# Kernel optimization log

Hardware: AMD Instinct MI355X
Metric: run time of the kernel (lower is better)

The kernel has to match this reference:

```python
import jax, jax.numpy as jnp
from jax import lax
import numpy as np


def conv4d(x, w, b, pad):
    """4D conv (stride 1) as a sum of 3D convs over the first-spatial-dim kernel taps.
    x: [B, Cin, T, D, H, W]; w: [Cout, Cin, Kt, Kd, Kh, Kw]; same pad on all dims."""
    B, Cin, T, D, H, W = x.shape
    Cout, _, Kt = w.shape[:3]
    xp = jnp.pad(x, ((0, 0), (0, 0), (pad, pad), (0, 0), (0, 0), (0, 0)))
    Tout = T + 2 * pad - Kt + 1
    acc = None
    for k in range(Kt):  # loop over kernel taps (<=3), not data dims
        xs = xp[:, :, k:k + Tout]                      # [B,Cin,Tout,D,H,W]
        xs = xs.transpose(0, 2, 1, 3, 4, 5).reshape(B * Tout, Cin, D, H, W)
        y = lax.conv_general_dilated(
            xs, w[:, :, k], (1, 1, 1), [(pad, pad)] * 3,
            dimension_numbers=('NCDHW', 'OIDHW', 'NCDHW'))
        acc = y if acc is None else acc + y
    Do, Ho, Wo = acc.shape[2:]
    out = acc.reshape(B, Tout, Cout, Do, Ho, Wo).transpose(0, 2, 1, 3, 4, 5)
    return out + b[None, :, None, None, None, None]


def tconv4d_k2s2(x, w, b):
    """4D transposed conv, kernel=2, stride=2, pad=0 (non-overlapping blocks).
    x: [B,Cin,T,D,H,W]; w: [Cin,Cout,2,2,2,2] (PyTorch ConvTranspose layout)."""
    B, Cin, T, D, H, W = x.shape
    Cout = w.shape[1]
    y = jnp.einsum('bcijkl,copqrs->boipjqkrls', x, w)
    y = y.reshape(B, Cout, 2 * T, 2 * D, 2 * H, 2 * W)
    return y + b[None, :, None, None, None, None]


def setup_inputs() -> dict:
    key = jax.random.key(0)
    ks = jax.random.split(key, 10)
    Cin, Cout = 64, 32
    x1 = jax.random.normal(ks[0], (2, Cin, 8, 8, 8, 8), dtype=jnp.float32)
    x2 = jax.random.normal(ks[1], (2, Cin // 2, 16, 16, 16, 16), dtype=jnp.float32)
    def w(k, shape, fan_in):
        return jax.random.normal(k, shape, dtype=jnp.float32) / np.float32(np.sqrt(fan_in))
    up_w = w(ks[2], (Cin, Cin // 2, 2, 2, 2, 2), Cin * 16)
    up_b = w(ks[3], (Cin // 2,), Cin * 16)
    w1 = w(ks[4], (Cout, Cin, 3, 3, 3, 3), Cin * 81)
    b1 = w(ks[5], (Cout,), Cin * 81)
    w2 = w(ks[6], (Cout, Cout, 3, 3, 3, 3), Cout * 81)
    b2 = w(ks[7], (Cout,), Cout * 81)
    w3 = w(ks[8], (Cout, Cin, 1, 1, 1, 1), Cin)
    b3 = w(ks[9], (Cout,), Cin)
    return {'x1': x1, 'x2': x2, 'up_w': up_w, 'up_b': up_b,
            'w1': w1, 'b1': b1, 'w2': w2, 'b2': b2, 'w3': w3, 'b3': b3}


def reference(x1, x2, up_w, up_b, w1, b1, w2, b2, w3, b3):
    x1u = tconv4d_k2s2(x1, up_w, up_b)              # [B, Cin//2, 16,16,16,16]
    xc = jnp.concatenate([x2, x1u], axis=1)          # [B, Cin, 16,16,16,16]
    Y = jax.nn.relu(conv4d(xc, w1, b1, 1))
    Y = conv4d(Y, w2, b2, 1)
    sc = conv4d(xc, w3, b3, 0)                       # 1x1 residual projection
    return jax.nn.relu(Y + sc)
```

## Files before the change

### kernel.cpp

```cpp
#include <hip/hip_runtime.h>

typedef unsigned short u16;
typedef __attribute__((ext_vector_type(8))) short short8;
typedef __attribute__((ext_vector_type(4))) float f32x4;

#define XCB_OFF  0
#define Y1B_OFF  8388608
#define W1P_OFF  12582912
#define W2P_OFF  12748800
#define W3P_OFF  12831744
#define UPWP_OFF 12833792

__device__ __forceinline__ u16 f2bf(float v) {
    unsigned u = __builtin_bit_cast(unsigned, v);
    u += 0x7FFFu + ((u >> 16) & 1u);
    return (u16)(u >> 16);
}

__device__ __forceinline__ f32x4 MFMA(short8 a, short8 b, f32x4 c) {
    return __builtin_amdgcn_mfma_f32_16x16x32_bf16(a, b, c, 0, 0, 0);
}

__device__ __forceinline__ void decode_bid(int bid, int& b, int& t, int& d, int& h0) {
    int xcd = bid & 7, loc = bid >> 3;
    int hB = loc & 1;
    d = (loc >> 1) & 15;
    int tsub = (loc >> 5) & 1;
    b = loc >> 6;
    t = xcd * 2 + tsub;
    h0 = hB * 8;
}

__global__ __launch_bounds__(256) void setup(const float* __restrict__ w1,
                                             const float* __restrict__ w2,
                                             const float* __restrict__ w3,
                                             const float* __restrict__ upw,
                                             const float* __restrict__ x2,
                                             u16* __restrict__ ws) {
    __shared__ u16 lds[256 * 40];
    int bid = blockIdx.x;
    int tid = threadIdx.x;
    if (bid < 512) {
        int b = bid >> 8;
        int pos_base = (bid & 255) * 256;
        u16* xcb = ws + XCB_OFF;
        #pragma unroll
        for (int c = 0; c < 32; ++c) {
            lds[tid * 40 + c] = f2bf(x2[((b * 32 + c) << 16) + pos_base + tid]);
        }
        __syncthreads();
        #pragma unroll
        for (int k = 0; k < 4; ++k) {
            int f = k * 256 + tid;
            int u = f & 3, pos = f >> 2;
            uint4 v = *(const uint4*)(lds + pos * 40 + u * 8);
            *(uint4*)(xcb + (size_t)((b << 16) + pos_base + pos) * 64 + u * 8) = v;
        }
    } else {
        int idx = (bid - 512) * 256 + tid;
        if (idx < 165888) {
            int j = idx & 7, lane = (idx >> 3) & 63, rest = idx >> 9;
            int half = rest & 1, chunk = (rest >> 1) & 1, tap = rest >> 2;
            int co = half * 16 + (lane & 15), ci = chunk * 32 + (lane >> 4) * 8 + j;
            ws[W1P_OFF + idx] = f2bf(w1[(co * 64 + ci) * 81 + tap]);
        } else if (idx < 165888 + 82944) {
            int i2 = idx - 165888;
            int j = i2 & 7, lane = (i2 >> 3) & 63, rest = i2 >> 9;
            int half = rest & 1, tap = rest >> 1;
            int co = half * 16 + (lane & 15), ci = (lane >> 4) * 8 + j;
            ws[W2P_OFF + i2] = f2bf(w2[(co * 32 + ci) * 81 + tap]);
        } else if (idx < 165888 + 82944 + 2048) {
            int i3 = idx - (165888 + 82944);
            int j = i3 & 7, lane = (i3 >> 3) & 63, rest = i3 >> 9;
            int half = rest & 1, chunk = rest >> 1;
            int co = half * 16 + (lane & 15), ci = chunk * 32 + (lane >> 4) * 8 + j;
            ws[W3P_OFF + i3] = f2bf(w3[co * 64 + ci]);
        } else if (idx < 250880 + 32768) {
            int i4 = idx - 250880;
            int j = i4 & 7, lane = (i4 >> 3) & 63, rest = i4 >> 9;
            int half = rest & 1, chunk = (rest >> 1) & 1, tap = rest >> 2;
            int co = half * 16 + (lane & 15), ci = chunk * 32 + (lane >> 4) * 8 + j;
            ws[UPWP_OFF + i4] = f2bf(upw[(ci * 32 + co) * 16 + tap]);
        }
    }
}

__global__ __launch_bounds__(256) void xc_up_mfma(const float* __restrict__ x1,
                                                  const u16* __restrict__ upwp,
                                                  const float* __restrict__ up_b,
                                                  u16* __restrict__ xcb) {
    __shared__ u16 lds[64 * 72];
    int tid = threadIdx.x;
    int wv = tid >> 6, lane = tid & 63;
    int q = lane >> 4, m = lane & 15;
    int bid = blockIdx.x;
    int j = bid & 63, b = bid >> 6;
    int pos_base = j * 64;

    #pragma unroll
    for (int g = 0; g < 16; ++g) {
        int c = g * 4 + wv;
        lds[lane * 72 + c] = f2bf(x1[((b * 64 + c) << 12) + pos_base + lane]);
    }
    __syncthreads();

    const short8* wv8 = (const short8*)upwp;
    float4 bi0 = ((const float4*)up_b)[q];
    float4 bi1 = ((const float4*)up_b)[4 + q];
    int it = j >> 3, id = j & 7;

    for (int tt = 0; tt < 4; ++tt) {
        int tap = wv * 4 + tt;
        f32x4 acc[4][2];
        #pragma unroll
        for (int g = 0; g < 4; ++g) {
            acc[g][0] = (f32x4){bi0.x, bi0.y, bi0.z, bi0.w};
            acc[g][1] = (f32x4){bi1.x, bi1.y, bi1.z, bi1.w};
        }
        #pragma unroll
        for (int chunk = 0; chunk < 2; ++chunk) {
            short8 a0 = wv8[((tap * 2 + chunk) * 2 + 0) * 64 + lane];
            short8 a1 = wv8[((tap * 2 + chunk) * 2 + 1) * 64 + lane];
            #pragma unroll
            for (int g = 0; g < 4; ++g) {
                short8 bf = *(const short8*)(lds + (g * 16 + m) * 72 + chunk * 32 + q * 8);
                acc[g][0] = MFMA(a0, bf, acc[g][0]);
                acc[g][1] = MFMA(a1, bf, acc[g][1]);
            }
        }
        int pt = tap >> 3, pd = (tap >> 2) & 1, ph = (tap >> 1) & 1, pw = tap & 1;
        int oT = 2 * it + pt, oD = 2 * id + pd, oW = 2 * (m & 7) + pw;
        #pragma unroll
        for (int g = 0; g < 4; ++g) {
            int ih = g * 2 + (m >> 3);
            int opos = oT * 4096 + oD * 256 + (2 * ih + ph) * 16 + oW;
            u16* op = xcb + (size_t)((b << 16) + opos) * 64 + 32 + q * 4;
            #pragma unroll
            for (int half = 0; half < 2; ++half) {
                f32x4 v = acc[g][half];
                uint2 o;
                o.x = (unsigned)f2bf(v.x) | ((unsigned)f2bf(v.y) << 16);
                o.y = (unsigned)f2bf(v.z) | ((unsigned)f2bf(v.w) << 16);
                *(uint2*)(op + half * 16) = o;
            }
        }
    }
}

__global__ __launch_bounds__(256, 4) void conv1_mfma(const u16* __restrict__ xcb,
                                                     const u16* __restrict__ w1p,
                                                     const float* __restrict__ b1,
                                                     u16* __restrict__ y1b) {
    __shared__ u16 lds[11520];
    int tid = threadIdx.x;
    int lane = tid & 63, wv = tid >> 6;
    int q = lane >> 4, m = lane & 15;
    int c = wv & 1, rg = wv >> 1;
    int b, t, d, h0;
    decode_bid(blockIdx.x, b, t, d, h0);
    int rot = (blockIdx.x * 5) % 9;

    int lofs[6], gofs[6];
    bool st[6], inr[6];
    #pragma unroll
    for (int k = 0; k < 6; ++k) {
        int ui = tid + k * 256;
        int u = ui & 7, p = (ui >> 3) % 18, hh = ui / 144;
        int gh = h0 - 1 + hh, gw = p - 1;
        st[k] = ui < 1440;
        inr[k] = st[k] && ((unsigned)gh < 16u) && ((unsigned)gw < 16u);
        gofs[k] = (gh * 16 + gw) * 64 + u * 8;
        lofs[k] = hh * 1152 + p * 64 + ((u ^ (p & 7)) * 8);
    }

    f32x4 acc[4][2];
    if (c == 0) {
        float4 bi0 = ((const float4*)b1)[q];
        float4 bi1 = ((const float4*)b1)[4 + q];
        #pragma unroll
        for (int i = 0; i < 4; ++i) {
            acc[i][0] = (f32x4){bi0.x, bi0.y, bi0.z, bi0.w};
            acc[i][1] = (f32x4){bi1.x, bi1.y, bi1.z, bi1.w};
        }
    } else {
        #pragma unroll
        for (int i = 0; i < 4; ++i) {
            acc[i][0] = (f32x4){0.f, 0.f, 0.f, 0.f};
            acc[i][1] = (f32x4){0.f, 0.f, 0.f, 0.f};
        }
    }
    const short8* w1v = (const short8*)w1p;

    uint4 rP[6];
    auto load_plane = [&](int ktd) {
        int kt = ktd / 3, kd = ktd - kt * 3;
        int tt = t + kt - 1, dd = d + kd - 1;
        bool pv = ((unsigned)tt < 16u) && ((unsigned)dd < 16u);
        const u16* src = xcb + (size_t)(((b * 16 + tt) * 16 + dd)) * 16384;
        #pragma unroll
        for (int k = 0; k < 6; ++k) {
            uint4 v = {0, 0, 0, 0};
            if (pv && inr[k]) v = *(const uint4*)(src + gofs[k]);
            rP[k] = v;
        }
    };
    auto write_plane = [&]() {
        #pragma unroll
        for (int k = 0; k < 6; ++k)
            if (st[k]) *(uint4*)(lds + lofs[k]) = rP[k];
    };

    load_plane(rot);
    for (int s = 0; s < 9; ++s) {
        int ktd = rot + s; if (ktd >= 9) ktd -= 9;
        __syncthreads();
        write_plane();
        if (s < 8) {
            int nk = ktd + 1; if (nk >= 9) nk -= 9;
            load_plane(nk);
        }
        __syncthreads();
        __builtin_amdgcn_s_setprio(1);
        #pragma unroll
        for (int kw = 0; kw < 3; ++kw) {
            int p = kw + m, pm = p & 7;
            int bo = p * 64 + ((((c << 2) | q) ^ pm) << 3);
            short8 R[6];
            #pragma unroll
            for (int r = 0; r < 6; ++r)
                R[r] = *(const short8*)(lds + (rg * 4 + r) * 1152 + bo);
            #pragma unroll
            for (int kh = 0; kh < 3; ++kh) {
                int tap = (ktd * 3 + kh) * 3 + kw;
                short8 a0 = w1v[((tap * 2 + c) * 2 + 0) * 64 + lane];
                short8 a1 = w1v[((tap * 2 + c) * 2 + 1) * 64 + lane];
                #pragma unroll
                for (int i = 0; i < 4; ++i) {
                    acc[i][0] = MFMA(a0, R[i + kh], acc[i][0]);
                    acc[i][1] = MFMA(a1, R[i + kh], acc[i][1]);
                }
            }
        }
        __builtin_amdgcn_s_setprio(0);
    }

    __syncthreads();
    f32x4* buf = (f32x4*)lds;
    if (c == 1) {
        #pragma unroll
        for (int i = 0; i < 4; ++i)
            #pragma unroll
            for (int half = 0; half < 2; ++half)
                buf[((rg * 4 + i) * 2 + half) * 64 + lane] = acc[i][half];
    }
    __syncthreads();
    if (c == 0) {
        int obase = ((b * 16 + t) * 16 + d) * 256 + (h0 + rg * 4) * 16 + m;
        #pragma unroll
        for (int i = 0; i < 4; ++i) {
            int pos = obase + i * 16;
            #pragma unroll
            for (int half = 0; half < 2; ++half) {
                f32x4 v = acc[i][half];
                f32x4 w = buf[((rg * 4 + i) * 2 + half) * 64 + lane];
                v.x += w.x; v.y += w.y; v.z += w.z; v.w += w.w;
                unsigned r0 = f2bf(fmaxf(v.x, 0.f)), r1 = f2bf(fmaxf(v.y, 0.f));
                unsigned r2 = f2bf(fmaxf(v.z, 0.f)), r3 = f2bf(fmaxf(v.w, 0.f));
                uint2 o;
                o.x = r0 | (r1 << 16);
                o.y = r2 | (r3 << 16);
                *(uint2*)(y1b + (size_t)pos * 32 + half * 16 + q * 4) = o;
            }
        }
    }
}

__global__ __launch_bounds__(256, 4) void conv2_mfma(const u16* __restrict__ y1b,
                                                     const u16* __restrict__ xcb,
                                                     const u16* __restrict__ w2p,
                                                     const u16* __restrict__ w3p,
                                                     const float* __restrict__ b2,
                                                     const float* __restrict__ b3,
                                                     float* __restrict__ out) {
    __shared__ u16 lds[11520];
    int tid = threadIdx.x;
    int lane = tid & 63, wv = tid >> 6;
    int q = lane >> 4, m = lane & 15;
    int rg = wv;
    int b, t, d, h0;
    decode_bid(blockIdx.x, b, t, d, h0);
    int rot = (blockIdx.x * 5) % 9;

    int lofs[3], gofs[3];
    bool st[3], inr[3];
    #pragma unroll
    for (int k = 0; k < 3; ++k) {
        int ui = tid + k * 256;
        int u = ui & 3, p = (ui >> 2) % 18, hh = ui / 72;
        int gh = h0 - 1 + hh, gw = p - 1;
        st[k] = ui < 720;
        inr[k] = st[k] && ((unsigned)gh < 16u) && ((unsigned)gw < 16u);
        gofs[k] = (gh * 16 + gw) * 32 + u * 8;
        lofs[k] = hh * 576 + p * 32 + ((u ^ (p & 3)) * 8);
    }

    f32x4 acc[2][2];
    #pragma unroll
    for (int hf = 0; hf < 2; ++hf) {
        float4 p0 = ((const float4*)b2)[hf * 4 + q];
        float4 s0 = ((const float4*)b3)[hf * 4 + q];
        #pragma unroll
        for (int i = 0; i < 2; ++i)
            acc[i][hf] = (f32x4){p0.x + s0.x, p0.y + s0.y, p0.z + s0.z, p0.w + s0.w};
    }
    const short8* w2v = (const short8*)w2p;

    uint4 rP[3];
    auto load_plane = [&](int ktd) {
        int kt = ktd / 3, kd = ktd - kt * 3;
        int tt = t + kt - 1, dd = d + kd - 1;
        bool pv = ((unsigned)tt < 16u) && ((unsigned)dd < 16u);
        const u16* src = y1b + (size_t)(((b * 16 + tt) * 16 + dd)) * 8192;
        #pragma unroll
        for (int k = 0; k < 3; ++k) {
            uint4 v = {0, 0, 0, 0};
            if (pv && inr[k]) v = *(const uint4*)(src + gofs[k]);
            rP[k] = v;
        }
    };
    auto write_plane = [&](int bb) {
        #pragma unroll
        for (int k = 0; k < 3; ++k)
            if (st[k]) *(uint4*)(lds + bb * 5760 + lofs[k]) = rP[k];
    };

    load_plane(rot);
    write_plane(0);
    { int nk = rot + 1; if (nk >= 9) nk -= 9; load_plane(nk); }

    for (int s = 0; s < 9; ++s) {
        int ktd = rot + s; if (ktd >= 9) ktd -= 9;
        __syncthreads();
        const u16* L = lds + (s & 1) * 5760;
        __builtin_amdgcn_s_setprio(1);
        #pragma unroll
        for (int kw = 0; kw < 3; ++kw) {
            int p = kw + m, pm = p & 3;
            int bo = p * 32 + ((q ^ pm) << 3);
            short8 R[4];
            #pragma unroll
            for (int r = 0; r < 4; ++r)
                R[r] = *(const short8*)(L + (rg * 2 + r) * 576 + bo);
            #pragma unroll
            for (int kh = 0; kh < 3; ++kh) {
                int tap = (ktd * 3 + kh) * 3 + kw;
                short8 a0 = w2v[(tap * 2 + 0) * 64 + lane];
                short8 a1 = w2v[(tap * 2 + 1) * 64 + lane];
                #pragma unroll
                for (int i = 0; i < 2; ++i) {
                    acc[i][0] = MFMA(a0, R[i + kh], acc[i][0]);
                    acc[i][1] = MFMA(a1, R[i + kh], acc[i][1]);
                }
            }
        }
        __builtin_amdgcn_s_setprio(0);
        if (s < 8) {
            write_plane((s + 1) & 1);
            if (s < 7) {
                int nk = ktd + 2; if (nk >= 9) nk -= 9;
                load_plane(nk);
            }
        }
    }

    const short8* w3v = (const short8*)w3p;
    int lpos0 = (t * 16 + d) * 256 + (h0 + rg * 2) * 16 + m;
    int gpos0 = (b << 16) + lpos0;
    #pragma unroll
    for (int chunk = 0; chunk < 2; ++chunk) {
        short8 a0 = w3v[(chunk * 2 + 0) * 64 + lane];
        short8 a1 = w3v[(chunk * 2 + 1) * 64 + lane];
        #pragma unroll
        for (int i = 0; i < 2; ++i) {
            short8 bf = *(const short8*)(xcb + (size_t)(gpos0 + i * 16) * 64 + ((chunk << 2) | q) * 8);
            acc[i][0] = MFMA(a0, bf, acc[i][0]);
            acc[i][1] = MFMA(a1, bf, acc[i][1]);
        }
    }

    #pragma unroll
    for (int i = 0; i < 2; ++i) {
        int lpos = lpos0 + i * 16;
        #pragma unroll
        for (int hf = 0; hf < 2; ++hf) {
            f32x4 v = acc[i][hf];
            int co = hf * 16 + q * 4;
            float* op = out + (((size_t)(b * 32 + co)) << 16) + lpos;
            op[0ull << 16] = fmaxf(v.x, 0.f);
            op[1ull << 16] = fmaxf(v.y, 0.f);
            op[2ull << 16] = fmaxf(v.z, 0.f);
            op[3ull << 16] = fmaxf(v.w, 0.f);
        }
    }
}

extern "C" void kernel_launch(void* const* d_in, const int* in_sizes, int n_in,
                              void* d_out, int out_size, void* d_ws, size_t ws_size,
                              hipStream_t stream) {
    const float* x1   = (const float*)d_in[0];
    const float* x2   = (const float*)d_in[1];
    const float* up_w = (const float*)d_in[2];
    const float* up_b = (const float*)d_in[3];
    const float* w1   = (const float*)d_in[4];
    const float* b1   = (const float*)d_in[5];
    const float* w2   = (const float*)d_in[6];
    const float* b2   = (const float*)d_in[7];
    const float* w3   = (const float*)d_in[8];
    const float* b3   = (const float*)d_in[9];
    u16* ws  = (u16*)d_ws;
    float* out = (float*)d_out;

    setup<<<1620, 256, 0, stream>>>(w1, w2, w3, up_w, x2, ws);
    xc_up_mfma<<<128, 256, 0, stream>>>(x1, ws + UPWP_OFF, up_b, ws + XCB_OFF);
    conv1_mfma<<<1024, 256, 0, stream>>>(ws + XCB_OFF, ws + W1P_OFF, b1, ws + Y1B_OFF);
    conv2_mfma<<<1024, 256, 0, stream>>>(ws + Y1B_OFF, ws + XCB_OFF, ws + W2P_OFF,
                                         ws + W3P_OFF, b2, b3, out);
}
```

Baseline: 162.2 us.

## Shrink conv blocks to two waves with larger per-wave output tiles

```diff
diff --git a/kernel.cpp b/kernel.cpp
--- a/kernel.cpp
+++ b/kernel.cpp
@@ -147,24 +147,23 @@
     }
 }
 
-__global__ __launch_bounds__(256, 4) void conv1_mfma(const u16* __restrict__ xcb,
+__global__ __launch_bounds__(128, 2) void conv1_mfma(const u16* __restrict__ xcb,
                                                      const u16* __restrict__ w1p,
                                                      const float* __restrict__ b1,
                                                      u16* __restrict__ y1b) {
     __shared__ u16 lds[11520];
     int tid = threadIdx.x;
-    int lane = tid & 63, wv = tid >> 6;
+    int lane = tid & 63, c = tid >> 6;
     int q = lane >> 4, m = lane & 15;
-    int c = wv & 1, rg = wv >> 1;
     int b, t, d, h0;
     decode_bid(blockIdx.x, b, t, d, h0);
     int rot = (blockIdx.x * 5) % 9;
 
-    int lofs[6], gofs[6];
-    bool st[6], inr[6];
-    #pragma unroll
-    for (int k = 0; k < 6; ++k) {
-        int ui = tid + k * 256;
+    int lofs[12], gofs[12];
+    bool st[12], inr[12];
+    #pragma unroll
+    for (int k = 0; k < 12; ++k) {
+        int ui = tid + k * 128;
         int u = ui & 7, p = (ui >> 3) % 18, hh = ui / 144;
         int gh = h0 - 1 + hh, gw = p - 1;
         st[k] = ui < 1440;
@@ -173,32 +172,32 @@
         lofs[k] = hh * 1152 + p * 64 + ((u ^ (p & 7)) * 8);
     }
 
-    f32x4 acc[4][2];
+    f32x4 acc[8][2];
     if (c == 0) {
         float4 bi0 = ((const float4*)b1)[q];
         float4 bi1 = ((const float4*)b1)[4 + q];
         #pragma unroll
-        for (int i = 0; i < 4; ++i) {
+        for (int i = 0; i < 8; ++i) {
             acc[i][0] = (f32x4){bi0.x, bi0.y, bi0.z, bi0.w};
             acc[i][1] = (f32x4){bi1.x, bi1.y, bi1.z, bi1.w};
         }
     } else {
         #pragma unroll
-        for (int i = 0; i < 4; ++i) {
+        for (int i = 0; i < 8; ++i) {
             acc[i][0] = (f32x4){0.f, 0.f, 0.f, 0.f};
             acc[i][1] = (f32x4){0.f, 0.f, 0.f, 0.f};
         }
     }
     const short8* w1v = (const short8*)w1p;
 
-    uint4 rP[6];
+    uint4 rP[12];
     auto load_plane = [&](int ktd) {
         int kt = ktd / 3, kd = ktd - kt * 3;
         int tt = t + kt - 1, dd = d + kd - 1;
         bool pv = ((unsigned)tt < 16u) && ((unsigned)dd < 16u);
         const u16* src = xcb + (size_t)(((b * 16 + tt) * 16 + dd)) * 16384;
         #pragma unroll
-        for (int k = 0; k < 6; ++k) {
+        for (int k = 0; k < 12; ++k) {
             uint4 v = {0, 0, 0, 0};
             if (pv && inr[k]) v = *(const uint4*)(src + gofs[k]);
             rP[k] = v;
@@ -206,7 +205,7 @@
     };
     auto write_plane = [&]() {
         #pragma unroll
-        for (int k = 0; k < 6; ++k)
+        for (int k = 0; k < 12; ++k)
             if (st[k]) *(uint4*)(lds + lofs[k]) = rP[k];
     };
 
@@ -225,17 +224,17 @@
         for (int kw = 0; kw < 3; ++kw) {
             int p = kw + m, pm = p & 7;
             int bo = p * 64 + ((((c << 2) | q) ^ pm) << 3);
-            short8 R[6];
-            #pragma unroll
-            for (int r = 0; r < 6; ++r)
-                R[r] = *(const short8*)(lds + (rg * 4 + r) * 1152 + bo);
+            short8 R[10];
+            #pragma unroll
+            for (int r = 0; r < 10; ++r)
+                R[r] = *(const short8*)(lds + r * 1152 + bo);
             #pragma unroll
             for (int kh = 0; kh < 3; ++kh) {
                 int tap = (ktd * 3 + kh) * 3 + kw;
                 short8 a0 = w1v[((tap * 2 + c) * 2 + 0) * 64 + lane];
                 short8 a1 = w1v[((tap * 2 + c) * 2 + 1) * 64 + lane];
                 #pragma unroll
-                for (int i = 0; i < 4; ++i) {
+                for (int i = 0; i < 8; ++i) {
                     acc[i][0] = MFMA(a0, R[i + kh], acc[i][0]);
                     acc[i][1] = MFMA(a1, R[i + kh], acc[i][1]);
                 }
@@ -248,21 +247,21 @@
     f32x4* buf = (f32x4*)lds;
     if (c == 1) {
         #pragma unroll
-        for (int i = 0; i < 4; ++i)
+        for (int i = 0; i < 8; ++i)
             #pragma unroll
             for (int half = 0; half < 2; ++half)
-                buf[((rg * 4 + i) * 2 + half) * 64 + lane] = acc[i][half];
+                buf[(i * 2 + half) * 64 + lane] = acc[i][half];
     }
     __syncthreads();
     if (c == 0) {
-        int obase = ((b * 16 + t) * 16 + d) * 256 + (h0 + rg * 4) * 16 + m;
-        #pragma unroll
-        for (int i = 0; i < 4; ++i) {
+        int obase = ((b * 16 + t) * 16 + d) * 256 + h0 * 16 + m;
+        #pragma unroll
+        for (int i = 0; i < 8; ++i) {
             int pos = obase + i * 16;
             #pragma unroll
             for (int half = 0; half < 2; ++half) {
                 f32x4 v = acc[i][half];
-                f32x4 w = buf[((rg * 4 + i) * 2 + half) * 64 + lane];
+                f32x4 w = buf[(i * 2 + half) * 64 + lane];
                 v.x += w.x; v.y += w.y; v.z += w.z; v.w += w.w;
                 unsigned r0 = f2bf(fmaxf(v.x, 0.f)), r1 = f2bf(fmaxf(v.y, 0.f));
                 unsigned r2 = f2bf(fmaxf(v.z, 0.f)), r3 = f2bf(fmaxf(v.w, 0.f));
@@ -275,113 +274,111 @@
     }
 }
 
-__global__ __launch_bounds__(256, 4) void conv2_mfma(const u16* __restrict__ y1b,
+__global__ __launch_bounds__(128, 2) void conv2_mfma(const u16* __restrict__ y1b,
                                                      const u16* __restrict__ xcb,
                                                      const u16* __restrict__ w2p,
                                                      const u16* __restrict__ w3p,
                                                      const float* __restrict__ b2,
                                                      const float* __restrict__ b3,
                                                      float* __restrict__ out) {
-    __shared__ u16 lds[11520];
+    __shared__ u16 lds[10368];
     int tid = threadIdx.x;
-    int lane = tid & 63, wv = tid >> 6;
+    int lane = tid & 63, rg = tid >> 6;
     int q = lane >> 4, m = lane & 15;
-    int rg = wv;
-    int b, t, d, h0;
-    decode_bid(blockIdx.x, b, t, d, h0);
-    int rot = (blockIdx.x * 5) % 9;
-
-    int lofs[3], gofs[3];
-    bool st[3], inr[3];
-    #pragma unroll
-    for (int k = 0; k < 3; ++k) {
-        int ui = tid + k * 256;
+    int bid = blockIdx.x;
+    int xcd = bid & 7, loc = bid >> 3;
+    int d = loc & 15;
+    int tsub = (loc >> 4) & 1;
+    int b = loc >> 5;
+    int t = xcd * 2 + tsub;
+    int rot = (bid * 5) % 9;
+
+    int lofs[11], gofs[11];
+    bool st[11], inr[11];
+    #pragma unroll
+    for (int k = 0; k < 11; ++k) {
+        int ui = tid + k * 128;
         int u = ui & 3, p = (ui >> 2) % 18, hh = ui / 72;
-        int gh = h0 - 1 + hh, gw = p - 1;
-        st[k] = ui < 720;
+        int gh = hh - 1, gw = p - 1;
+        st[k] = ui < 1296;
         inr[k] = st[k] && ((unsigned)gh < 16u) && ((unsigned)gw < 16u);
         gofs[k] = (gh * 16 + gw) * 32 + u * 8;
         lofs[k] = hh * 576 + p * 32 + ((u ^ (p & 3)) * 8);
     }
 
-    f32x4 acc[2][2];
+    f32x4 acc[8][2];
     #pragma unroll
     for (int hf = 0; hf < 2; ++hf) {
         float4 p0 = ((const float4*)b2)[hf * 4 + q];
         float4 s0 = ((const float4*)b3)[hf * 4 + q];
         #pragma unroll
-        for (int i = 0; i < 2; ++i)
+        for (int i = 0; i < 8; ++i)
             acc[i][hf] = (f32x4){p0.x + s0.x, p0.y + s0.y, p0.z + s0.z, p0.w + s0.w};
     }
     const short8* w2v = (const short8*)w2p;
 
-    uint4 rP[3];
+    uint4 rP[11];
     auto load_plane = [&](int ktd) {
         int kt = ktd / 3, kd = ktd - kt * 3;
         int tt = t + kt - 1, dd = d + kd - 1;
         bool pv = ((unsigned)tt < 16u) && ((unsigned)dd < 16u);
         const u16* src = y1b + (size_t)(((b * 16 + tt) * 16 + dd)) * 8192;
         #pragma unroll
-        for (int k = 0; k < 3; ++k) {
+        for (int k = 0; k < 11; ++k) {
             uint4 v = {0, 0, 0, 0};
             if (pv && inr[k]) v = *(const uint4*)(src + gofs[k]);
             rP[k] = v;
         }
     };
-    auto write_plane = [&](int bb) {
-        #pragma unroll
-        for (int k = 0; k < 3; ++k)
-            if (st[k]) *(uint4*)(lds + bb * 5760 + lofs[k]) = rP[k];
+    auto write_plane = [&]() {
+        #pragma unroll
+        for (int k = 0; k < 11; ++k)
+            if (st[k]) *(uint4*)(lds + lofs[k]) = rP[k];
     };
 
     load_plane(rot);
-    write_plane(0);
-    { int nk = rot + 1; if (nk >= 9) nk -= 9; load_plane(nk); }
-
     for (int s = 0; s < 9; ++s) {
         int ktd = rot + s; if (ktd >= 9) ktd -= 9;
         __syncthreads();
-        const u16* L = lds + (s & 1) * 5760;
+        write_plane();
+        if (s < 8) {
+            int nk = ktd + 1; if (nk >= 9) nk -= 9;
+            load_plane(nk);
+        }
+        __syncthreads();
         __builtin_amdgcn_s_setprio(1);
         #pragma unroll
         for (int kw = 0; kw < 3; ++kw) {
             int p = kw + m, pm = p & 3;
             int bo = p * 32 + ((q ^ pm) << 3);
-            short8 R[4];
-            #pragma unroll
-            for (int r = 0; r < 4; ++r)
-                R[r] = *(const short8*)(L + (rg * 2 + r) * 576 + bo);
+            short8 R[10];
+            #pragma unroll
+            for (int r = 0; r < 10; ++r)
+                R[r] = *(const short8*)(lds + (rg * 8 + r) * 576 + bo);
             #pragma unroll
             for (int kh = 0; kh < 3; ++kh) {
                 int tap = (ktd * 3 + kh) * 3 + kw;
                 short8 a0 = w2v[(tap * 2 + 0) * 64 + lane];
                 short8 a1 = w2v[(tap * 2 + 1) * 64 + lane];
                 #pragma unroll
-                for (int i = 0; i < 2; ++i) {
+                for (int i = 0; i < 8; ++i) {
                     acc[i][0] = MFMA(a0, R[i + kh], acc[i][0]);
                     acc[i][1] = MFMA(a1, R[i + kh], acc[i][1]);
                 }
             }
         }
         __builtin_amdgcn_s_setprio(0);
-        if (s < 8) {
-            write_plane((s + 1) & 1);
-            if (s < 7) {
-                int nk = ktd + 2; if (nk >= 9) nk -= 9;
-                load_plane(nk);
-            }
-        }
     }
 
     const short8* w3v = (const short8*)w3p;
-    int lpos0 = (t * 16 + d) * 256 + (h0 + rg * 2) * 16 + m;
+    int lpos0 = (t * 16 + d) * 256 + (rg * 8) * 16 + m;
     int gpos0 = (b << 16) + lpos0;
     #pragma unroll
     for (int chunk = 0; chunk < 2; ++chunk) {
         short8 a0 = w3v[(chunk * 2 + 0) * 64 + lane];
         short8 a1 = w3v[(chunk * 2 + 1) * 64 + lane];
         #pragma unroll
-        for (int i = 0; i < 2; ++i) {
+        for (int i = 0; i < 8; ++i) {
             short8 bf = *(const short8*)(xcb + (size_t)(gpos0 + i * 16) * 64 + ((chunk << 2) | q) * 8);
             acc[i][0] = MFMA(a0, bf, acc[i][0]);
             acc[i][1] = MFMA(a1, bf, acc[i][1]);
@@ -389,7 +386,7 @@
     }
 
     #pragma unroll
-    for (int i = 0; i < 2; ++i) {
+    for (int i = 0; i < 8; ++i) {
         int lpos = lpos0 + i * 16;
         #pragma unroll
         for (int hf = 0; hf < 2; ++hf) {
@@ -422,7 +419,7 @@
 
     setup<<<1620, 256, 0, stream>>>(w1, w2, w3, up_w, x2, ws);
     xc_up_mfma<<<128, 256, 0, stream>>>(x1, ws + UPWP_OFF, up_b, ws + XCB_OFF);
-    conv1_mfma<<<1024, 256, 0, stream>>>(ws + XCB_OFF, ws + W1P_OFF, b1, ws + Y1B_OFF);
-    conv2_mfma<<<1024, 256, 0, stream>>>(ws + Y1B_OFF, ws + XCB_OFF, ws + W2P_OFF,
-                                         ws + W3P_OFF, b2, b3, out);
-}
+    conv1_mfma<<<1024, 128, 0, stream>>>(ws + XCB_OFF, ws + W1P_OFF, b1, ws + Y1B_OFF);
+    conv2_mfma<<<512, 128, 0, stream>>>(ws + Y1B_OFF, ws + XCB_OFF, ws + W2P_OFF,
+                                        ws + W3P_OFF, b2, b3, out);
+}
```

Result: slower. 168.9 us (+4.1%).
